# Kernel optimization log

Measured on AMD Instinct MI355X. Metric: run time of the kernel, lower is better.

The kernel has to match this reference:

```python
import jax, jax.numpy as jnp
import numpy as np


def _lsap_np(cost):
    """Jonker-Volgenant / Hungarian (e-maxx formulation) for a square cost
    matrix. Returns col_of_row: row i is assigned to column col_of_row[i].
    Matches scipy.optimize.linear_sum_assignment on square matrices."""
    cost = np.asarray(cost, dtype=np.float64)
    n = cost.shape[0]
    u = np.zeros(n + 1)
    v = np.zeros(n + 1)
    p = np.zeros(n + 1, dtype=np.int64)   # p[j] = row assigned to column j (1-based; 0 = none)
    way = np.zeros(n + 1, dtype=np.int64)
    for i in range(1, n + 1):
        p[0] = i
        j0 = 0
        minv = np.full(n + 1, np.inf)
        used = np.zeros(n + 1, dtype=bool)
        while True:
            used[j0] = True
            i0 = p[j0]
            js = np.nonzero(~used[1:])[0] + 1  # unused columns (vectorized inner loop)
            cur = cost[i0 - 1, js - 1] - u[i0] - v[js]
            better = cur < minv[js]
            minv[js] = np.where(better, cur, minv[js])
            way[js] = np.where(better, j0, way[js])
            j1 = js[np.argmin(minv[js])]
            delta = minv[j1]
            u[p[used]] += delta          # rows assigned to used columns are distinct
            v[used] -= delta
            minv[~used] -= delta
            j0 = j1
            if p[j0] == 0:
                break
        # augment along the alternating path
        while j0 != 0:
            j1 = way[j0]
            p[j0] = p[j1]
            j0 = j1
    col_of_row = np.zeros(n, dtype=np.int32)
    for j in range(1, n + 1):
        if p[j] > 0:
            col_of_row[p[j] - 1] = j - 1
    return col_of_row


def _batched_lsap_host(dists):
    dists = np.asarray(dists)
    return np.stack([_lsap_np(d) for d in dists]).astype(np.int32)  # [B, N]


def _pairwise_dist(y_true, y_pred):
    # dist[b, i, j] = || y_true[b, i] - y_pred[b, j] ||_2, matching tf.norm(..., axis=-1)
    diff = y_true[:, :, None, :] - y_pred[:, None, :, :]  # [B, N, N, D]
    return jnp.sqrt(jnp.sum(diff * diff, axis=-1))        # [B, N, N]


def setup_inputs() -> dict:
    key = jax.random.key(0)
    k1, k2 = jax.random.split(key)
    B, N, D = 64, 128, 64
    y_true = jax.random.normal(k1, (B, N, D), dtype=jnp.float32)
    y_pred = jax.random.normal(k2, (B, N, D), dtype=jnp.float32)
    return {"y_true": y_true, "y_pred": y_pred}


def reference(y_true, y_pred):
    dist = _pairwise_dist(y_true, y_pred)                      # [B, N, N]
    B, N = dist.shape[0], dist.shape[1]
    col_ind = jax.pure_callback(
        _batched_lsap_host,
        jax.ShapeDtypeStruct((B, N), jnp.int32),
        jax.lax.stop_gradient(dist),
    )                                                          # [B, N]
    matched = jnp.take_along_axis(dist, col_ind[:, :, None].astype(jnp.int32), axis=2)[..., 0]
    batch_losses = jnp.sum(matched, axis=1)                    # [B]
    return jnp.mean(batch_losses)
```

## Files before the change

kernel.cpp:

```cpp
#include <hip/hip_runtime.h>
#include <math.h>
#include <stdint.h>

#define BATCH 64
#define N 128
#define DIM 64
#define ARR_CAP 384

typedef unsigned uint32x2_t __attribute__((ext_vector_type(2)));

__device__ __forceinline__ unsigned monokey(float x) {
    unsigned b = __float_as_uint(x);
    return b ^ (unsigned)(((int)b >> 31) | (int)0x80000000u);
}

__device__ __forceinline__ unsigned umin_(unsigned a, unsigned b) { return a < b ? a : b; }
__device__ __forceinline__ unsigned umax_(unsigned a, unsigned b) { return a > b ? a : b; }
__device__ __forceinline__ int rl_i(int v, int l) { return __builtin_amdgcn_readlane(v, l); }
__device__ __forceinline__ float rl_f(float v, int l) {
    return __int_as_float(__builtin_amdgcn_readlane(__float_as_int(v), l));
}

#define DPP_ROR(x, n) __builtin_amdgcn_update_dpp((int)(x), (int)(x), 0x120 + (n), 0xF, 0xF, false)

__device__ __forceinline__ unsigned partner16(unsigned x, int lane) {
#if __has_builtin(__builtin_amdgcn_permlane16_swap)
    uint32x2_t r = __builtin_amdgcn_permlane16_swap(x, x, false, false);
    return (lane & 16) ? r[0] : r[1];
#else
    return (unsigned)__shfl_xor((int)x, 16);
#endif
}
__device__ __forceinline__ unsigned partner32(unsigned x, int lane) {
#if __has_builtin(__builtin_amdgcn_permlane32_swap)
    uint32x2_t r = __builtin_amdgcn_permlane32_swap(x, x, false, false);
    return (lane & 32) ? r[0] : r[1];
#else
    return (unsigned)__shfl_xor((int)x, 32);
#endif
}

__device__ __forceinline__ unsigned wave_kmin(unsigned k) {
    unsigned a = (unsigned)DPP_ROR(k, 1);
    unsigned b = (unsigned)DPP_ROR(k, 2);
    k = umin_(k, umin_(a, b));
    a = (unsigned)DPP_ROR(k, 3);
    b = (unsigned)DPP_ROR(k, 6);
    k = umin_(k, umin_(a, b));
    a = (unsigned)DPP_ROR(k, 9);
    k = umin_(k, a);
#if __has_builtin(__builtin_amdgcn_permlane16_swap)
    {
        uint32x2_t r = __builtin_amdgcn_permlane16_swap(k, k, false, false);
        k = umin_(r[0], r[1]);
    }
#else
    k = umin_(k, (unsigned)__shfl_xor((int)k, 16));
#endif
#if __has_builtin(__builtin_amdgcn_permlane32_swap)
    {
        uint32x2_t r = __builtin_amdgcn_permlane32_swap(k, k, false, false);
        k = umin_(r[0], r[1]);
    }
#else
    k = umin_(k, (unsigned)__shfl_xor((int)k, 32));
#endif
    return k;
}

__device__ __forceinline__ void wave_kmin2(unsigned& ks, unsigned& kb, int lane) {
    unsigned ps, pb;
#define KM2_COMBINE { unsigned ns = umin_(ks, ps); kb = umin_(umin_(kb, pb), umax_(ks, ps)); ks = ns; }
    ps = (unsigned)DPP_ROR(ks, 1); pb = (unsigned)DPP_ROR(kb, 1); KM2_COMBINE;
    ps = (unsigned)DPP_ROR(ks, 2); pb = (unsigned)DPP_ROR(kb, 2); KM2_COMBINE;
    ps = (unsigned)DPP_ROR(ks, 4); pb = (unsigned)DPP_ROR(kb, 4); KM2_COMBINE;
    ps = (unsigned)DPP_ROR(ks, 8); pb = (unsigned)DPP_ROR(kb, 8); KM2_COMBINE;
    ps = partner16(ks, lane); pb = partner16(kb, lane); KM2_COMBINE;
    ps = partner32(ks, lane); pb = partner32(kb, lane); KM2_COMBINE;
#undef KM2_COMBINE
}

__global__ __launch_bounds__(64, 1)
void lsap_kernel(const float* __restrict__ y_true, const float* __restrict__ y_pred,
                 float* __restrict__ batch_sums, float* __restrict__ out, int use_atomic) {
    __shared__ float dist[N * N];
    __shared__ float ytl[N * DIM];
    __shared__ long long pu[N + 1];
    __shared__ int way[N + 1];
    __shared__ float u_row[N];
    __shared__ int unlist[N + ARR_CAP + 4];

    const int b = blockIdx.x;
    const int lane = threadIdx.x;
    const int ca = lane, cb = lane + 64;
    const int ja = lane + 1, jb = lane + 65;

    {
        const float4* yt4 = (const float4*)(y_true + (size_t)b * N * DIM);
        float4* ytl4 = (float4*)ytl;
        for (int k = lane; k < N * DIM / 4; k += 64) ytl4[k] = yt4[k];
    }

    float ypa[DIM], ypb[DIM];
    {
        const float4* pa4 = (const float4*)(y_pred + (size_t)b * N * DIM + (size_t)ca * DIM);
        const float4* pb4 = (const float4*)(y_pred + (size_t)b * N * DIM + (size_t)cb * DIM);
        #pragma unroll
        for (int k = 0; k < DIM / 4; ++k) {
            float4 v4 = pa4[k];
            ypa[4*k+0]=v4.x; ypa[4*k+1]=v4.y; ypa[4*k+2]=v4.z; ypa[4*k+3]=v4.w;
            float4 w4 = pb4[k];
            ypb[4*k+0]=w4.x; ypb[4*k+1]=w4.y; ypb[4*k+2]=w4.z; ypb[4*k+3]=w4.w;
        }
    }

    pu[ja] = 0; pu[jb] = 0;
    if (lane == 0) pu[0] = 0;
    __syncthreads();

    float va = INFINITY, vb = INFINITY;
    for (int i = 0; i < N; ++i) {
        const float4* yr = (const float4*)(ytl + i * DIM);
        float a0 = 0.f, a1 = 0.f;
        #pragma unroll
        for (int k = 0; k < DIM / 4; ++k) {
            float4 t4 = yr[k];
            float d;
            d = t4.x - ypa[4*k+0]; a0 = fmaf(d, d, a0);
            d = t4.y - ypa[4*k+1]; a0 = fmaf(d, d, a0);
            d = t4.z - ypa[4*k+2]; a0 = fmaf(d, d, a0);
            d = t4.w - ypa[4*k+3]; a0 = fmaf(d, d, a0);
            d = t4.x - ypb[4*k+0]; a1 = fmaf(d, d, a1);
            d = t4.y - ypb[4*k+1]; a1 = fmaf(d, d, a1);
            d = t4.z - ypb[4*k+2]; a1 = fmaf(d, d, a1);
            d = t4.w - ypb[4*k+3]; a1 = fmaf(d, d, a1);
        }
        float d0 = sqrtf(a0), d1 = sqrtf(a1);
        dist[i * N + ca] = d0;
        dist[i * N + cb] = d1;
        va = fminf(va, d0);
        vb = fminf(vb, d1);
    }

    int nun = 0;
    for (int r = 0; r < N; ++r) {
        float c0 = dist[r * N + ca] - va;
        float c1 = dist[r * N + cb] - vb;
        float cand = fminf(c0, c1);
        int colm = (c0 <= c1) ? ja : jb;
        unsigned key = (monokey(cand) & ~63u) | (unsigned)lane;
        key = wave_kmin(key);
        int w = (int)(__builtin_amdgcn_readfirstlane((int)key) & 63);
        float g = rl_f(cand, w);
        int js = rl_i(colm, w);
        int owner = (int)pu[js];
        if (lane == 0) u_row[r] = g;
        if (owner == 0) {
            if (lane == 0) pu[js] = ((long long)__float_as_int(g) << 32) | (unsigned)(r + 1);
        } else {
            if (lane == 0) unlist[nun] = r;
            ++nun;
        }
    }

    int k = 0, nf = nun, ops = 0, pending = -1;
    while (ops < ARR_CAP) {
        int i;
        if (pending >= 0) { i = pending; pending = -1; }
        else if (k < nf) { i = unlist[k]; ++k; }
        else break;
        ++ops;

        float c0 = dist[i * N + ca] - va;
        float c1 = dist[i * N + cb] - vb;
        unsigned k0 = (monokey(c0) & ~63u) | (unsigned)lane;
        unsigned k1 = (monokey(c1) & ~63u) | (unsigned)lane;
        bool afirst = (k0 <= k1);
        unsigned ks = afirst ? k0 : k1, kb = afirst ? k1 : k0;
        float sm = afirst ? c0 : c1, bg = afirst ? c1 : c0;
        int colm = afirst ? ja : jb, colS = afirst ? jb : ja;
        wave_kmin2(ks, kb, lane);
        int w1 = (int)(__builtin_amdgcn_readfirstlane((int)ks) & 63);
        int w2 = (int)(__builtin_amdgcn_readfirstlane((int)kb) & 63);
        float u1 = rl_f(sm, w1);
        int j1 = rl_i(colm, w1);
        float u2; int j2;
        if (w2 == w1) { u2 = rl_f(bg, w1); j2 = rl_i(colS, w1); }
        else          { u2 = rl_f(sm, w2); j2 = rl_i(colm, w2); }

        long long q1 = pu[j1];
        long long q2 = pu[j2];
        int i0 = (int)q1;
        int jt, it0;
        if (u1 < u2) {
            float dd = u2 - u1;
            if (ja == j1) va -= dd;
            if (jb == j1) vb -= dd;
            jt = j1; it0 = i0;
        } else if (i0 > 0) {
            jt = j2; it0 = (int)q2;
        } else {
            jt = j1; it0 = 0;
        }
        if (lane == 0) {
            pu[jt] = ((long long)__float_as_int(u2) << 32) | (unsigned)(i + 1);
            u_row[i] = u2;
        }
        if (it0 > 0) {
            if (u1 < u2) pending = it0 - 1;
            else { if (lane == 0) unlist[nf] = it0 - 1; ++nf; }
        }
    }
    if (pending >= 0) { --k; if (lane == 0) unlist[k] = pending; }
    __syncthreads();

    for (int t = k; t < nf; ++t) {
        int r = unlist[t];
        long long ta = pu[ja], tb = pu[jb];
        int pa = (int)ta, pb = (int)tb;
        float upa = __int_as_float((int)(ta >> 32));
        float upb = __int_as_float((int)(tb >> 32));
        float mina = INFINITY, minb = INFINITY;
        int useda = 0, usedb = 0, waya = 0, wayb = 0;
        float uacca = 0.f, uaccb = 0.f;
        const float u_i = u_row[r];
        float u_acc_i = u_i;
        int j0 = 0, i0 = r + 1;
        float u0c = u_i;

        for (;;) {
            if (ja == j0) useda = 1;
            if (jb == j0) usedb = 1;
            const float* drow = dist + (i0 - 1) * N;
            float d0 = drow[ca], d1 = drow[cb];
            if (!useda) { float cur = d0 - u0c - va; if (cur < mina) { mina = cur; waya = j0; } }
            if (!usedb) { float cur = d1 - u0c - vb; if (cur < minb) { minb = cur; wayb = j0; } }

            float cand = useda ? INFINITY : mina;
            int cm = ja, pm = pa; float um = upa;
            float candb = usedb ? INFINITY : minb;
            if (candb < cand) { cand = candb; cm = jb; pm = pb; um = upb; }

            unsigned key = (monokey(cand) & ~63u) | (unsigned)lane;
            key = wave_kmin(key);
            int w = (int)(__builtin_amdgcn_readfirstlane((int)key) & 63);
            float delta = rl_f(cand, w);
            int pkj = rl_i((pm << 8) | cm, w);
            float u1v = rl_f(um, w);

            if (useda) { va -= delta; uacca += delta; } else { mina -= delta; }
            if (usedb) { vb -= delta; uaccb += delta; } else { minb -= delta; }
            u_acc_i += delta;

            j0 = pkj & 255;
            int i1 = pkj >> 8;
            if (i1 == 0) break;
            i0 = i1; u0c = u1v;
        }

        way[ja] = waya; way[jb] = wayb;
        {
            int* pui = (int*)pu;
            if (useda) pui[2 * ja + 1] = __float_as_int(upa + uacca);
            if (usedb) pui[2 * jb + 1] = __float_as_int(upb + uaccb);
        }
        __syncthreads();
        if (lane == 0) {
            int jj = j0;
            for (;;) {
                int jp = way[jj];
                if (jp == 0) {
                    pu[jj] = ((long long)__float_as_int(u_acc_i) << 32) | (unsigned)(r + 1);
                    break;
                }
                pu[jj] = pu[jp];
                jj = jp;
            }
        }
        __syncthreads();
    }
    __syncthreads();

    long long ta = pu[ja], tb = pu[jb];
    int pa = (int)ta, pb = (int)tb;
    float s = dist[(pa - 1) * N + ca] + dist[(pb - 1) * N + cb];
    #pragma unroll
    for (int m = 1; m < 64; m <<= 1) s += __shfl_xor(s, m);
    if (lane == 0) {
        if (use_atomic) atomicAdd(out, s * (1.0f / (float)BATCH));
        else batch_sums[b] = s;
    }
}

__global__ __launch_bounds__(64)
void reduce_kernel(const float* __restrict__ bs, float* __restrict__ out) {
    int tid = threadIdx.x;
    float v = bs[tid];
    #pragma unroll
    for (int m = 1; m < 64; m <<= 1) v += __shfl_xor(v, m);
    if (tid == 0) out[0] = v * (1.0f / (float)BATCH);
}

extern "C" void kernel_launch(void* const* d_in, const int* in_sizes, int n_in,
                              void* d_out, int out_size, void* d_ws, size_t ws_size,
                              hipStream_t stream) {
    const float* y_true = (const float*)d_in[0];
    const float* y_pred = (const float*)d_in[1];
    float* out = (float*)d_out;

    if (ws_size >= BATCH * sizeof(float)) {
        float* bs = (float*)d_ws;
        lsap_kernel<<<BATCH, 64, 0, stream>>>(y_true, y_pred, bs, out, 0);
        reduce_kernel<<<1, 64, 0, stream>>>(bs, out);
    } else {
        hipMemsetAsync(d_out, 0, sizeof(float), stream);
        lsap_kernel<<<BATCH, 64, 0, stream>>>(y_true, y_pred, nullptr, out, 1);
    }
}
```

Measured before the change: 587.2 us.

## Keep Hungarian assignment state in registers and decode values from reduction keys

Moves the column-to-row assignment, column potentials, row potentials and way arrays out of LDS and into per-lane registers, reading them back with readlane. The augmenting-path walk then runs wave-uniformly instead of on lane 0 between barriers. Reduction keys now carry the half-selector bit, so the minimum value and column come straight out of the key rather than from extra readlanes. Initial row assignment uses a two-minimum reduction, and the auction cap rises to 640. This removes LDS round-trips and syncthreads from the serial loop. In exchange, the low key bits are truncated, which quantises the decoded values and could change tie-breaking.

```diff
diff --git a/kernel.cpp b/kernel.cpp
--- a/kernel.cpp
+++ b/kernel.cpp
@@ -5,13 +5,17 @@
 #define BATCH 64
 #define N 128
 #define DIM 64
-#define ARR_CAP 384
+#define ARR_CAP 640
 
 typedef unsigned uint32x2_t __attribute__((ext_vector_type(2)));
 
 __device__ __forceinline__ unsigned monokey(float x) {
     unsigned b = __float_as_uint(x);
     return b ^ (unsigned)(((int)b >> 31) | (int)0x80000000u);
+}
+__device__ __forceinline__ float monoval(unsigned k) {
+    unsigned b = (k & 0x80000000u) ? (k & 0x7FFFFFFFu) : ~k;
+    return __uint_as_float(b);
 }
 
 __device__ __forceinline__ unsigned umin_(unsigned a, unsigned b) { return a < b ? a : b; }
@@ -23,20 +27,20 @@
 
 #define DPP_ROR(x, n) __builtin_amdgcn_update_dpp((int)(x), (int)(x), 0x120 + (n), 0xF, 0xF, false)
 
-__device__ __forceinline__ unsigned partner16(unsigned x, int lane) {
+__device__ __forceinline__ unsigned partner16(unsigned x) {
 #if __has_builtin(__builtin_amdgcn_permlane16_swap)
     uint32x2_t r = __builtin_amdgcn_permlane16_swap(x, x, false, false);
-    return (lane & 16) ? r[0] : r[1];
+    return umin_(r[0], r[1]);
 #else
-    return (unsigned)__shfl_xor((int)x, 16);
+    return umin_(x, (unsigned)__shfl_xor((int)x, 16));
 #endif
 }
-__device__ __forceinline__ unsigned partner32(unsigned x, int lane) {
+__device__ __forceinline__ unsigned partner32(unsigned x) {
 #if __has_builtin(__builtin_amdgcn_permlane32_swap)
     uint32x2_t r = __builtin_amdgcn_permlane32_swap(x, x, false, false);
-    return (lane & 32) ? r[0] : r[1];
+    return umin_(r[0], r[1]);
 #else
-    return (unsigned)__shfl_xor((int)x, 32);
+    return umin_(x, (unsigned)__shfl_xor((int)x, 32));
 #endif
 }
 
@@ -49,35 +53,39 @@
     k = umin_(k, umin_(a, b));
     a = (unsigned)DPP_ROR(k, 9);
     k = umin_(k, a);
-#if __has_builtin(__builtin_amdgcn_permlane16_swap)
-    {
-        uint32x2_t r = __builtin_amdgcn_permlane16_swap(k, k, false, false);
-        k = umin_(r[0], r[1]);
-    }
-#else
-    k = umin_(k, (unsigned)__shfl_xor((int)k, 16));
-#endif
-#if __has_builtin(__builtin_amdgcn_permlane32_swap)
-    {
-        uint32x2_t r = __builtin_amdgcn_permlane32_swap(k, k, false, false);
-        k = umin_(r[0], r[1]);
-    }
-#else
-    k = umin_(k, (unsigned)__shfl_xor((int)k, 32));
-#endif
+    k = partner16(k);
+    k = partner32(k);
     return k;
 }
 
 __device__ __forceinline__ void wave_kmin2(unsigned& ks, unsigned& kb, int lane) {
     unsigned ps, pb;
 #define KM2_COMBINE { unsigned ns = umin_(ks, ps); kb = umin_(umin_(kb, pb), umax_(ks, ps)); ks = ns; }
+#define KM2_SWAP16 { \
+    uint32x2_t rs = __builtin_amdgcn_permlane16_swap(ks, ks, false, false); \
+    uint32x2_t rb = __builtin_amdgcn_permlane16_swap(kb, kb, false, false); \
+    ps = (lane & 16) ? rs[0] : rs[1]; pb = (lane & 16) ? rb[0] : rb[1]; }
+#define KM2_SWAP32 { \
+    uint32x2_t rs = __builtin_amdgcn_permlane32_swap(ks, ks, false, false); \
+    uint32x2_t rb = __builtin_amdgcn_permlane32_swap(kb, kb, false, false); \
+    ps = (lane & 32) ? rs[0] : rs[1]; pb = (lane & 32) ? rb[0] : rb[1]; }
     ps = (unsigned)DPP_ROR(ks, 1); pb = (unsigned)DPP_ROR(kb, 1); KM2_COMBINE;
     ps = (unsigned)DPP_ROR(ks, 2); pb = (unsigned)DPP_ROR(kb, 2); KM2_COMBINE;
     ps = (unsigned)DPP_ROR(ks, 4); pb = (unsigned)DPP_ROR(kb, 4); KM2_COMBINE;
     ps = (unsigned)DPP_ROR(ks, 8); pb = (unsigned)DPP_ROR(kb, 8); KM2_COMBINE;
-    ps = partner16(ks, lane); pb = partner16(kb, lane); KM2_COMBINE;
-    ps = partner32(ks, lane); pb = partner32(kb, lane); KM2_COMBINE;
+#if __has_builtin(__builtin_amdgcn_permlane16_swap)
+    KM2_SWAP16; KM2_COMBINE;
+#else
+    ps = (unsigned)__shfl_xor((int)ks, 16); pb = (unsigned)__shfl_xor((int)kb, 16); KM2_COMBINE;
+#endif
+#if __has_builtin(__builtin_amdgcn_permlane32_swap)
+    KM2_SWAP32; KM2_COMBINE;
+#else
+    ps = (unsigned)__shfl_xor((int)ks, 32); pb = (unsigned)__shfl_xor((int)kb, 32); KM2_COMBINE;
+#endif
 #undef KM2_COMBINE
+#undef KM2_SWAP16
+#undef KM2_SWAP32
 }
 
 __global__ __launch_bounds__(64, 1)
@@ -85,10 +93,7 @@
                  float* __restrict__ batch_sums, float* __restrict__ out, int use_atomic) {
     __shared__ float dist[N * N];
     __shared__ float ytl[N * DIM];
-    __shared__ long long pu[N + 1];
-    __shared__ int way[N + 1];
-    __shared__ float u_row[N];
-    __shared__ int unlist[N + ARR_CAP + 4];
+    __shared__ int unlist[N + ARR_CAP + 8];
 
     const int b = blockIdx.x;
     const int lane = threadIdx.x;
@@ -113,9 +118,6 @@
             ypb[4*k+0]=w4.x; ypb[4*k+1]=w4.y; ypb[4*k+2]=w4.z; ypb[4*k+3]=w4.w;
         }
     }
-
-    pu[ja] = 0; pu[jb] = 0;
-    if (lane == 0) pu[0] = 0;
     __syncthreads();
 
     float va = INFINITY, vb = INFINITY;
@@ -142,93 +144,100 @@
         vb = fminf(vb, d1);
     }
 
+    int   pa = 0, pb = 0;
+    float upa = 0.f, upb = 0.f;
+    float ura = 0.f, urb = 0.f;
+    int   waya = 0, wayb = 0;
+
     int nun = 0;
     for (int r = 0; r < N; ++r) {
         float c0 = dist[r * N + ca] - va;
         float c1 = dist[r * N + cb] - vb;
-        float cand = fminf(c0, c1);
-        int colm = (c0 <= c1) ? ja : jb;
-        unsigned key = (monokey(cand) & ~63u) | (unsigned)lane;
-        key = wave_kmin(key);
-        int w = (int)(__builtin_amdgcn_readfirstlane((int)key) & 63);
-        float g = rl_f(cand, w);
-        int js = rl_i(colm, w);
-        int owner = (int)pu[js];
-        if (lane == 0) u_row[r] = g;
-        if (owner == 0) {
-            if (lane == 0) pu[js] = ((long long)__float_as_int(g) << 32) | (unsigned)(r + 1);
+        unsigned k0 = (monokey(c0) & ~0x7Fu) | (unsigned)lane;
+        unsigned k1 = (monokey(c1) & ~0x7Fu) | 64u | (unsigned)lane;
+        unsigned ks = umin_(k0, k1), kb2 = umax_(k0, k1);
+        wave_kmin2(ks, kb2, lane);
+        int s1 = __builtin_amdgcn_readfirstlane((int)ks);
+        int s2 = __builtin_amdgcn_readfirstlane((int)kb2);
+        float u1 = monoval((unsigned)s1 & ~0x7Fu);
+        float u2 = monoval((unsigned)s2 & ~0x7Fu);
+        int w1 = s1 & 63, cb1 = (s1 >> 6) & 1;
+        int j1 = 1 + w1 + (cb1 << 6);
+        int pj1 = rl_i(cb1 ? pb : pa, w1);
+        if (pj1 == 0) {
+            float dd = u2 - u1;
+            if (ja == j1) { pa = r + 1; upa = u2; va -= dd; }
+            if (jb == j1) { pb = r + 1; upb = u2; vb -= dd; }
+            if ((r & 63) == lane) { if (r < 64) ura = u2; else urb = u2; }
         } else {
-            if (lane == 0) unlist[nun] = r;
+            unlist[nun] = r;
             ++nun;
+            if ((r & 63) == lane) { if (r < 64) ura = u1; else urb = u1; }
         }
     }
 
     int k = 0, nf = nun, ops = 0, pending = -1;
+    int unext = unlist[0];
     while (ops < ARR_CAP) {
         int i;
         if (pending >= 0) { i = pending; pending = -1; }
-        else if (k < nf) { i = unlist[k]; ++k; }
+        else if (k < nf) { i = unext; ++k; unext = unlist[k]; }
         else break;
         ++ops;
 
         float c0 = dist[i * N + ca] - va;
         float c1 = dist[i * N + cb] - vb;
-        unsigned k0 = (monokey(c0) & ~63u) | (unsigned)lane;
-        unsigned k1 = (monokey(c1) & ~63u) | (unsigned)lane;
-        bool afirst = (k0 <= k1);
-        unsigned ks = afirst ? k0 : k1, kb = afirst ? k1 : k0;
-        float sm = afirst ? c0 : c1, bg = afirst ? c1 : c0;
-        int colm = afirst ? ja : jb, colS = afirst ? jb : ja;
-        wave_kmin2(ks, kb, lane);
-        int w1 = (int)(__builtin_amdgcn_readfirstlane((int)ks) & 63);
-        int w2 = (int)(__builtin_amdgcn_readfirstlane((int)kb) & 63);
-        float u1 = rl_f(sm, w1);
-        int j1 = rl_i(colm, w1);
-        float u2; int j2;
-        if (w2 == w1) { u2 = rl_f(bg, w1); j2 = rl_i(colS, w1); }
-        else          { u2 = rl_f(sm, w2); j2 = rl_i(colm, w2); }
-
-        long long q1 = pu[j1];
-        long long q2 = pu[j2];
-        int i0 = (int)q1;
+        unsigned k0 = (monokey(c0) & ~0x7Fu) | (unsigned)lane;
+        unsigned k1 = (monokey(c1) & ~0x7Fu) | 64u | (unsigned)lane;
+        unsigned ks = umin_(k0, k1), kb2 = umax_(k0, k1);
+        wave_kmin2(ks, kb2, lane);
+        int s1 = __builtin_amdgcn_readfirstlane((int)ks);
+        int s2 = __builtin_amdgcn_readfirstlane((int)kb2);
+        float u1 = monoval((unsigned)s1 & ~0x7Fu);
+        float u2 = monoval((unsigned)s2 & ~0x7Fu);
+        int w1 = s1 & 63, cb1 = (s1 >> 6) & 1;
+        int w2 = s2 & 63, cb2 = (s2 >> 6) & 1;
+        int j1 = 1 + w1 + (cb1 << 6);
+        int j2 = 1 + w2 + (cb2 << 6);
+        int pj1 = rl_i(cb1 ? pb : pa, w1);
+        int pj2 = rl_i(cb2 ? pb : pa, w2);
+
         int jt, it0;
         if (u1 < u2) {
             float dd = u2 - u1;
             if (ja == j1) va -= dd;
             if (jb == j1) vb -= dd;
-            jt = j1; it0 = i0;
-        } else if (i0 > 0) {
-            jt = j2; it0 = (int)q2;
-        } else {
-            jt = j1; it0 = 0;
-        }
-        if (lane == 0) {
-            pu[jt] = ((long long)__float_as_int(u2) << 32) | (unsigned)(i + 1);
-            u_row[i] = u2;
-        }
+            jt = j1; it0 = pj1;
+        } else if (pj1 > 0) { jt = j2; it0 = pj2; }
+        else { jt = j1; it0 = 0; }
+
+        if (ja == jt) { pa = i + 1; upa = u2; }
+        if (jb == jt) { pb = i + 1; upb = u2; }
+        if ((i & 63) == lane) { if (i < 64) ura = u2; else urb = u2; }
+
         if (it0 > 0) {
             if (u1 < u2) pending = it0 - 1;
-            else { if (lane == 0) unlist[nf] = it0 - 1; ++nf; }
-        }
-    }
-    if (pending >= 0) { --k; if (lane == 0) unlist[k] = pending; }
-    __syncthreads();
+            else {
+                unlist[nf] = it0 - 1;
+                if (k == nf) unext = it0 - 1;
+                ++nf;
+            }
+        }
+    }
+    if (pending >= 0) { --k; unlist[k] = pending; }
 
     for (int t = k; t < nf; ++t) {
         int r = unlist[t];
-        long long ta = pu[ja], tb = pu[jb];
-        int pa = (int)ta, pb = (int)tb;
-        float upa = __int_as_float((int)(ta >> 32));
-        float upb = __int_as_float((int)(tb >> 32));
+        float u_i = rl_f((r >= 64) ? urb : ura, r & 63);
         float mina = INFINITY, minb = INFINITY;
-        int useda = 0, usedb = 0, waya = 0, wayb = 0;
+        int useda = 0, usedb = 0;
+        waya = 0; wayb = 0;
         float uacca = 0.f, uaccb = 0.f;
-        const float u_i = u_row[r];
         float u_acc_i = u_i;
         int j0 = 0, i0 = r + 1;
         float u0c = u_i;
 
-        for (;;) {
+        for (int it = 0; it < N + 1; ++it) {
             if (ja == j0) useda = 1;
             if (jb == j0) usedb = 1;
             const float* drow = dist + (i0 - 1) * N;
@@ -236,53 +245,50 @@
             if (!useda) { float cur = d0 - u0c - va; if (cur < mina) { mina = cur; waya = j0; } }
             if (!usedb) { float cur = d1 - u0c - vb; if (cur < minb) { minb = cur; wayb = j0; } }
 
-            float cand = useda ? INFINITY : mina;
-            int cm = ja, pm = pa; float um = upa;
-            float candb = usedb ? INFINITY : minb;
-            if (candb < cand) { cand = candb; cm = jb; pm = pb; um = upb; }
-
-            unsigned key = (monokey(cand) & ~63u) | (unsigned)lane;
-            key = wave_kmin(key);
-            int w = (int)(__builtin_amdgcn_readfirstlane((int)key) & 63);
-            float delta = rl_f(cand, w);
-            int pkj = rl_i((pm << 8) | cm, w);
-            float u1v = rl_f(um, w);
+            float candA = useda ? INFINITY : mina;
+            float candB = usedb ? INFINITY : minb;
+            unsigned kA = (monokey(candA) & ~0x7Fu) | (unsigned)lane;
+            unsigned kB = (monokey(candB) & ~0x7Fu) | 64u | (unsigned)lane;
+            unsigned kk = wave_kmin(umin_(kA, kB));
+            int s = __builtin_amdgcn_readfirstlane((int)kk);
+            float delta = monoval((unsigned)s & ~0x7Fu);
+            int w = s & 63, cbw = (s >> 6) & 1;
+            int j1 = 1 + w + (cbw << 6);
+            int i1 = rl_i(cbw ? pb : pa, w);
+            float u1v = rl_f(cbw ? upb : upa, w);
 
             if (useda) { va -= delta; uacca += delta; } else { mina -= delta; }
             if (usedb) { vb -= delta; uaccb += delta; } else { minb -= delta; }
             u_acc_i += delta;
 
-            j0 = pkj & 255;
-            int i1 = pkj >> 8;
+            j0 = j1;
             if (i1 == 0) break;
             i0 = i1; u0c = u1v;
         }
 
-        way[ja] = waya; way[jb] = wayb;
-        {
-            int* pui = (int*)pu;
-            if (useda) pui[2 * ja + 1] = __float_as_int(upa + uacca);
-            if (usedb) pui[2 * jb + 1] = __float_as_int(upb + uaccb);
-        }
-        __syncthreads();
-        if (lane == 0) {
-            int jj = j0;
-            for (;;) {
-                int jp = way[jj];
-                if (jp == 0) {
-                    pu[jj] = ((long long)__float_as_int(u_acc_i) << 32) | (unsigned)(r + 1);
-                    break;
-                }
-                pu[jj] = pu[jp];
-                jj = jp;
+        if (useda) upa += uacca;
+        if (usedb) upb += uaccb;
+
+        int jj = j0;
+        for (int hop = 0; hop < N + 1; ++hop) {
+            int wj = (jj - 1) & 63;
+            int sbj = (jj > 64) ? 1 : 0;
+            int jp = rl_i(sbj ? wayb : waya, wj);
+            int np; float nu;
+            if (jp == 0) { np = r + 1; nu = u_acc_i; }
+            else {
+                int wp = (jp - 1) & 63;
+                int sbp = (jp > 64) ? 1 : 0;
+                np = rl_i(sbp ? pb : pa, wp);
+                nu = rl_f(sbp ? upb : upa, wp);
             }
-        }
-        __syncthreads();
-    }
-    __syncthreads();
-
-    long long ta = pu[ja], tb = pu[jb];
-    int pa = (int)ta, pb = (int)tb;
+            if (ja == jj) { pa = np; upa = nu; }
+            if (jb == jj) { pb = np; upb = nu; }
+            if (jp == 0) break;
+            jj = jp;
+        }
+    }
+
     float s = dist[(pa - 1) * N + ca] + dist[(pb - 1) * N + cb];
     #pragma unroll
     for (int m = 1; m < 64; m <<= 1) s += __shfl_xor(s, m);
```

Measured after the change: 594.8 us. Within noise of the previous version (+1.3%).
